# Kernel tuning notes

Hardware: AMD Instinct MI355X
Metric: run time of the kernel (lower is better)

Reference implementation:

```python
import jax, jax.numpy as jnp
import numpy as np
import math

NUM_HEADS = 12


def setup_inputs() -> dict:
    key = jax.random.key(0)
    ks = jax.random.split(key, 9)
    R, L, B, E = 128, 512, 1, 768
    s = 1.0 / math.sqrt(E)
    return {
        "x": jax.random.normal(ks[0], (R, L, B, E), dtype=jnp.float32),
        "wq": jax.random.normal(ks[1], (E, E), dtype=jnp.float32) * s,
        "bq": jax.random.normal(ks[2], (E,), dtype=jnp.float32) * 0.02,
        "wk": jax.random.normal(ks[3], (E, E), dtype=jnp.float32) * s,
        "bk": jax.random.normal(ks[4], (E,), dtype=jnp.float32) * 0.02,
        "wv": jax.random.normal(ks[5], (E, E), dtype=jnp.float32) * s,
        "bv": jax.random.normal(ks[6], (E,), dtype=jnp.float32) * 0.02,
        "wo": jax.random.normal(ks[7], (E, E), dtype=jnp.float32) * s,
        "bo": jax.random.normal(ks[8], (E,), dtype=jnp.float32) * 0.02,
    }


def reference(x, wq, bq, wk, bk, wv, bv, wo, bo):
    # x: [num_rows, num_cols, batch, embed_dim]
    R, L, B, E = x.shape
    H = NUM_HEADS
    D = E // H
    # scaling = head_dim**-0.5 / sqrt(num_rows)  (align_scaling)
    scaling = (D ** -0.5) / math.sqrt(R)

    q = (x @ wq.T + bq).reshape(R, L, B, H, D) * scaling
    k = (x @ wk.T + bk).reshape(R, L, B, H, D)
    v = (x @ wv.T + bv).reshape(R, L, B, H, D)

    # row attention: contract over rows r and head_dim d -> logits [h, n, i, j]
    attn_weights = jnp.einsum("rinhd,rjnhd->hnij", q, k)
    attn_probs = jax.nn.softmax(attn_weights, axis=-1)

    context = jnp.einsum("hnij,rjnhd->rinhd", attn_probs, v)
    context = context.reshape(R, L, B, E)
    output = context @ wo.T + bo
    return (output, attn_probs)
```

## Files before the change

kernel.cpp:

```cpp
#include <hip/hip_runtime.h>
#include <hip/hip_bf16.h>

typedef unsigned short u16;
typedef u16   u16x4 __attribute__((ext_vector_type(4)));
typedef u16   u16x8 __attribute__((ext_vector_type(8)));
typedef short bf16x8 __attribute__((ext_vector_type(8)));
typedef float f32x4 __attribute__((ext_vector_type(4)));

#define R_    128
#define L_    512
#define E_    768
#define H_    12
#define RD_   8192
#define M_    65536
#define OUT0_N 50331648
#define PART_ 3145728

__device__ __forceinline__ u16 rne_bf16(float f) {
  unsigned u = __builtin_bit_cast(unsigned, f);
  u += 0x7FFFu + ((u >> 16) & 1u);
  return (u16)(u >> 16);
}

__device__ __forceinline__ void gload_lds16(const u16* g, u16* l) {
  __builtin_amdgcn_global_load_lds(
      (const __attribute__((address_space(1))) void*)g,
      (__attribute__((address_space(3))) void*)l, 16, 0, 0);
}

__device__ __forceinline__ int xcd_remap(int d, int nwg) {
  return (d & 7) * (nwg >> 3) + (d >> 3);
}

__device__ __forceinline__ void gemm_core256(
    const u16* __restrict__ Ab, const u16* __restrict__ Bb,
    const int lda, const int ldb, const int K,
    u16* sm, f32x4 acc[8][4])
{
  const int t    = threadIdx.x;
  const int lane = t & 63;
  const int w    = t >> 6;
  const int wm   = (w >> 2) << 7;
  const int wn   = (w & 3) << 6;
  const int frow = lane & 15;

  const int srow  = t >> 2;
  const int gslot = (t & 3) ^ ((t >> 3) & 3);
  const u16* gA0 = Ab + (size_t)srow * lda + (gslot << 3);
  const u16* gA1 = Ab + (size_t)(srow + 128) * lda + (gslot << 3);
  const u16* gB0 = Bb + (size_t)srow * ldb + (gslot << 3);
  const u16* gB1 = Bb + (size_t)(srow + 128) * ldb + (gslot << 3);
  const int stg = t << 3;

  const int rdoff = (((lane >> 4) ^ ((lane >> 1) & 3)) << 3);

#define STAGE256(tt_, buf_)                                            \
  {                                                                    \
    const size_t ko_ = (size_t)(tt_) << 5;                             \
    gload_lds16(gA0 + ko_, (buf_) + stg);                              \
    gload_lds16(gA1 + ko_, (buf_) + 4096 + stg);                       \
    gload_lds16(gB0 + ko_, (buf_) + 8192 + stg);                       \
    gload_lds16(gB1 + ko_, (buf_) + 12288 + stg);                      \
  }

  const int nt = K >> 5;
  STAGE256(0, sm);
  asm volatile("s_waitcnt vmcnt(0)" ::: "memory");
  __builtin_amdgcn_s_barrier();

  for (int tt = 0; tt < nt; ++tt) {
    u16* bufc = sm + ((tt & 1) << 14);
    u16* bufn = sm + (((tt + 1) & 1) << 14);
    if (tt + 1 < nt) STAGE256(tt + 1, bufn);

    bf16x8 af[8], bff[4];
#pragma unroll
    for (int b = 0; b < 4; ++b)
      bff[b] = *(const bf16x8*)(bufc + 8192 + ((wn + b * 16 + frow) << 5) + rdoff);
#pragma unroll
    for (int a = 0; a < 8; ++a)
      af[a] = *(const bf16x8*)(bufc + ((wm + a * 16 + frow) << 5) + rdoff);

    __builtin_amdgcn_s_setprio(1);
#pragma unroll
    for (int a = 0; a < 8; ++a)
#pragma unroll
      for (int b = 0; b < 4; ++b)
        acc[a][b] = __builtin_amdgcn_mfma_f32_16x16x32_bf16(af[a], bff[b], acc[a][b], 0, 0, 0);
    __builtin_amdgcn_s_setprio(0);

    asm volatile("s_waitcnt vmcnt(0)" ::: "memory");
    __builtin_amdgcn_s_barrier();
  }
#undef STAGE256
}

#define EPILOGUE_IDX256                           \
  const int lane = threadIdx.x & 63;              \
  const int w    = threadIdx.x >> 6;              \
  const int wm   = (w >> 2) << 7;                 \
  const int wn   = (w & 3) << 6;                  \
  const int row4 = (lane >> 4) << 2;              \
  const int coll = lane & 15;

#define ACC_INIT256                               \
  f32x4 acc[8][4];                                \
  {                                               \
    f32x4 zz = {0.0f, 0.0f, 0.0f, 0.0f};          \
    _Pragma("unroll")                             \
    for (int a = 0; a < 8; ++a)                   \
      _Pragma("unroll")                           \
      for (int b = 0; b < 4; ++b) acc[a][b] = zz; \
  }

__device__ __forceinline__ void gemm_core(
    const u16* __restrict__ Ab, const u16* __restrict__ Bb,
    const int lda, const int ldb, const int K,
    u16* sm, f32x4 acc[4][4])
{
  const int t    = threadIdx.x;
  const int lane = t & 63;
  const int w    = t >> 6;
  const int wm   = (w >> 1) << 6;
  const int wn   = (w & 1) << 6;
  const int frow = lane & 15;

  const int srow = (w << 3) + (lane >> 3);
  const int scol = ((lane & 7) ^ (lane >> 3)) << 3;
  const u16* gA = Ab + (size_t)srow * lda + scol;
  const u16* gB = Bb + (size_t)srow * ldb + scol;
  const int stg_l = (w << 9) + (lane << 3);

#pragma unroll
  for (int j = 0; j < 4; ++j) {
    gload_lds16(gA + (size_t)(j << 5) * lda, sm + (j << 11) + stg_l);
    gload_lds16(gB + (size_t)(j << 5) * ldb, sm + 8192 + (j << 11) + stg_l);
  }

  const int nt = K >> 6;
  for (int tt = 0; tt < nt; ++tt) {
    const int cur = tt & 1;
    u16* bufc = sm + (cur << 14);
    u16* bufn = sm + ((cur ^ 1) << 14);
    __builtin_amdgcn_s_barrier();
    if (tt + 1 < nt) {
      const u16* gA1 = gA + ((size_t)(tt + 1) << 6);
      const u16* gB1 = gB + ((size_t)(tt + 1) << 6);
#pragma unroll
      for (int j = 0; j < 4; ++j) {
        gload_lds16(gA1 + (size_t)(j << 5) * lda, bufn + (j << 11) + stg_l);
        gload_lds16(gB1 + (size_t)(j << 5) * ldb, bufn + 8192 + (j << 11) + stg_l);
      }
      asm volatile("s_waitcnt vmcnt(8)" ::: "memory");
    } else {
      asm volatile("s_waitcnt vmcnt(0)" ::: "memory");
    }
    __builtin_amdgcn_s_barrier();
    const u16* sA = bufc;
    const u16* sB = bufc + 8192;
#pragma unroll
    for (int kk = 0; kk < 2; ++kk) {
      const int rdcol = (((kk << 2) + (lane >> 4)) ^ (lane & 7)) << 3;
      bf16x8 af[4], bff[4];
#pragma unroll
      for (int a = 0; a < 4; ++a)
        af[a] = *(const bf16x8*)(sA + ((wm + a * 16 + frow) << 6) + rdcol);
#pragma unroll
      for (int b = 0; b < 4; ++b)
        bff[b] = *(const bf16x8*)(sB + ((wn + b * 16 + frow) << 6) + rdcol);
#pragma unroll
      for (int a = 0; a < 4; ++a)
#pragma unroll
        for (int b = 0; b < 4; ++b)
          acc[a][b] = __builtin_amdgcn_mfma_f32_16x16x32_bf16(af[a], bff[b], acc[a][b], 0, 0, 0);
    }
  }
}

#define EPILOGUE_IDX                              \
  const int lane = threadIdx.x & 63;              \
  const int w    = threadIdx.x >> 6;              \
  const int wm   = (w >> 1) << 6;                 \
  const int wn   = (w & 1) << 6;                  \
  const int row4 = (lane >> 4) << 2;              \
  const int coll = lane & 15;

#define ACC_INIT                                  \
  f32x4 acc[4][4];                                \
  {                                               \
    f32x4 zz = {0.0f, 0.0f, 0.0f, 0.0f};          \
    _Pragma("unroll")                             \
    for (int a = 0; a < 4; ++a)                   \
      _Pragma("unroll")                           \
      for (int b = 0; b < 4; ++b) acc[a][b] = zz; \
  }

__global__ __launch_bounds__(512) void k_gemm_qkv(
    const u16* __restrict__ xbf, const u16* __restrict__ wqkv,
    const float* __restrict__ bq, const float* __restrict__ bk,
    const float* __restrict__ bv,
    u16* __restrict__ qt, u16* __restrict__ kt, u16* __restrict__ vt2,
    const float scaling)
{
  __shared__ __align__(16) u16 smem[32768];
  const int d0 = blockIdx.x + 9 * blockIdx.y;
  const int l  = xcd_remap(d0, 2304);
  const int bn = l % 9;
  const int bm = l / 9;
  ACC_INIT256;
  gemm_core256(xbf + (size_t)bm * 256 * E_, wqkv + (size_t)bn * 256 * E_,
               E_, E_, E_, smem, acc);
  EPILOGUE_IDX256;
  const int which = bn / 3;
  const int c0 = (bn % 3) << 8;
  const float* bias = (which == 0) ? bq : (which == 1) ? bk : bv;

  if (which < 2) {
    u16* dst = (which == 0) ? qt : kt;
    const float mult = (which == 0) ? scaling : 1.0f;
#pragma unroll
    for (int a = 0; a < 8; ++a) {
#pragma unroll
      for (int b = 0; b < 4; ++b) {
        const int c = c0 + wn + b * 16 + coll;
        const int h = c >> 6, d = c & 63;
        const float bias_v = bias[c];
#pragma unroll
        for (int r = 0; r < 4; ++r) {
          const int m = (bm << 8) + wm + a * 16 + row4 + r;
          const int rr = m >> 9, i = m & 511;
          const float v = (acc[a][b][r] + bias_v) * mult;
          dst[((size_t)(h * 512 + i) << 13) + (rr << 6) + d] = rne_bf16(v);
        }
      }
    }
  } else {
    const int rr = bm >> 1;
    const int j0 = (bm & 1) << 8;
    const int wq4 = w & 3;
    for (int p = 0; p < 4; ++p) {
      __syncthreads();
      if (wq4 == p) {
#pragma unroll
        for (int a = 0; a < 8; ++a) {
          const int ml = wm + a * 16 + row4;
#pragma unroll
          for (int b = 0; b < 4; ++b) {
            const int c = c0 + wn + b * 16 + coll;
            const int nl = b * 16 + coll;
            const float bias_v = bias[c];
            u16x4 pk;
#pragma unroll
            for (int r = 0; r < 4; ++r) pk[r] = rne_bf16(acc[a][b][r] + bias_v);
            *(u16x4*)(smem + nl * 264 + ml) = pk;
          }
        }
      }
      __syncthreads();
      for (int idx = threadIdx.x; idx < 2048; idx += 512) {
        const int nl = idx >> 5, seg = idx & 31;
        const int c = c0 + (p << 6) + nl;
        const int h = c >> 6, d = c & 63;
        u16x8 vdat = *(const u16x8*)(smem + nl * 264 + (seg << 3));
        *(u16x8*)(vt2 + ((size_t)((h << 13) + (rr << 6) + d) << 9) + j0 + (seg << 3)) = vdat;
      }
    }
  }
}

__global__ __launch_bounds__(256) void k_gemm_logits(
    const u16* __restrict__ qt, const u16* __restrict__ kt,
    float* __restrict__ lgp)
{
  __shared__ __align__(16) u16 smem[32768];
  const int d0 = blockIdx.x + 4 * blockIdx.y + 16 * blockIdx.z;
  const int l  = xcd_remap(d0, 768);
  const int bm = l & 3, bn = (l >> 2) & 3;
  const int hk = l >> 4;
  const int h  = hk >> 2, ks = hk & 3;
  ACC_INIT;
  const u16* A = qt + ((size_t)h << 22) + ((size_t)bm << 20) + (ks << 11);
  const u16* B = kt + ((size_t)h << 22) + ((size_t)bn << 20) + (ks << 11);
  gemm_core(A, B, RD_, RD_, 2048, smem, acc);
  EPILOGUE_IDX;
  float* dst = lgp + ((size_t)(ks * 12 + h) << 18);
#pragma unroll
  for (int a = 0; a < 4; ++a)
#pragma unroll
    for (int b = 0; b < 4; ++b) {
      const int j = bn * 128 + wn + b * 16 + coll;
#pragma unroll
      for (int r = 0; r < 4; ++r) {
        const int i = bm * 128 + wm + a * 16 + row4 + r;
        dst[((size_t)i << 9) + j] = acc[a][b][r];
      }
    }
}

__global__ __launch_bounds__(256) void k_softmax(
    const float* __restrict__ lgp, float* __restrict__ probs,
    u16* __restrict__ pbf)
{
  const int row = blockIdx.x;
  const size_t base = (size_t)row << 9;
  const int t = threadIdx.x;
  const int lane = t & 63, w = t >> 6;
  float x0 = (lgp[base + t]       + lgp[PART_ + base + t])
           + (lgp[2 * (size_t)PART_ + base + t]       + lgp[3 * (size_t)PART_ + base + t]);
  float x1 = (lgp[base + t + 256] + lgp[PART_ + base + t + 256])
           + (lgp[2 * (size_t)PART_ + base + t + 256] + lgp[3 * (size_t)PART_ + base + t + 256]);
  float m = fmaxf(x0, x1);
#pragma unroll
  for (int off = 32; off > 0; off >>= 1) m = fmaxf(m, __shfl_xor(m, off, 64));
  __shared__ float red[8];
  if (lane == 0) red[w] = m;
  __syncthreads();
  m = fmaxf(fmaxf(red[0], red[1]), fmaxf(red[2], red[3]));
  float e0 = __expf(x0 - m), e1 = __expf(x1 - m);
  float s = e0 + e1;
#pragma unroll
  for (int off = 32; off > 0; off >>= 1) s += __shfl_xor(s, off, 64);
  if (lane == 0) red[4 + w] = s;
  __syncthreads();
  s = (red[4] + red[5]) + (red[6] + red[7]);
  const float inv = 1.0f / s;
  const float p0 = e0 * inv, p1 = e1 * inv;
  probs[base + t] = p0;
  probs[base + t + 256] = p1;
  pbf[base + t]       = rne_bf16(p0);
  pbf[base + t + 256] = rne_bf16(p1);
}

__global__ __launch_bounds__(512) void k_gemm_ctx(
    const u16* __restrict__ pbf, const u16* __restrict__ vt2,
    u16* __restrict__ ctx)
{
  __shared__ __align__(16) u16 smem[32768];
  const int d0 = blockIdx.x + (blockIdx.y << 6);
  const int l  = xcd_remap(d0, 768);
  const int bm = l & 1, bn = (l >> 1) & 31, h = l >> 6;
  ACC_INIT256;
  const u16* A = pbf + ((size_t)h << 18) + ((size_t)bm << 17);
  const u16* B = vt2 + ((size_t)h << 22) + ((size_t)bn << 17);
  gemm_core256(A, B, 512, 512, 512, smem, acc);
  EPILOGUE_IDX256;
#pragma unroll
  for (int a = 0; a < 8; ++a)
#pragma unroll
    for (int b = 0; b < 4; ++b) {
      const int n = (bn << 8) + wn + b * 16 + coll;
      const int rr = n >> 6, d = n & 63;
#pragma unroll
      for (int r = 0; r < 4; ++r) {
        const int i = (bm << 8) + wm + a * 16 + row4 + r;
        ctx[(size_t)((rr << 9) + i) * E_ + (h << 6) + d] = rne_bf16(acc[a][b][r]);
      }
    }
}

__global__ __launch_bounds__(512) void k_gemm_out(
    const u16* __restrict__ ctx, const u16* __restrict__ wob,
    const float* __restrict__ bo, float* __restrict__ out0)
{
  __shared__ __align__(16) u16 smem[32768];
  const int d0 = blockIdx.x + 3 * blockIdx.y;
  const int l  = xcd_remap(d0, 768);
  const int bn = l % 3;
  const int bm = l / 3;
  ACC_INIT256;
  gemm_core256(ctx + (size_t)bm * 256 * E_, wob + (size_t)bn * 256 * E_,
               E_, E_, E_, smem, acc);
  EPILOGUE_IDX256;
#pragma unroll
  for (int a = 0; a < 8; ++a)
#pragma unroll
    for (int b = 0; b < 4; ++b) {
      const int n = (bn << 8) + wn + b * 16 + coll;
      const float bias_v = bo[n];
#pragma unroll
      for (int r = 0; r < 4; ++r) {
        const int m = (bm << 8) + wm + a * 16 + row4 + r;
        out0[(size_t)m * E_ + n] = acc[a][b][r] + bias_v;
      }
    }
}

__device__ __forceinline__ u16x4 cvt4(float4 v) {
  u16x4 o;
  o.x = rne_bf16(v.x); o.y = rne_bf16(v.y);
  o.z = rne_bf16(v.z); o.w = rne_bf16(v.w);
  return o;
}

__global__ __launch_bounds__(256) void k_cvt_x(
    const float4* __restrict__ src, u16x4* __restrict__ dst, const int n4)
{
  const int stride = gridDim.x * blockDim.x;
  for (int i = blockIdx.x * blockDim.x + threadIdx.x; i < n4; i += stride)
    dst[i] = cvt4(src[i]);
}

__global__ __launch_bounds__(256) void k_cvt_w(
    const float4* __restrict__ wq, const float4* __restrict__ wk,
    const float4* __restrict__ wv, const float4* __restrict__ wo,
    u16x4* __restrict__ wqkv, u16x4* __restrict__ wob)
{
  const int n4 = (E_ * E_) / 4;
  const int stride = gridDim.x * blockDim.x;
  for (int i = blockIdx.x * blockDim.x + threadIdx.x; i < n4; i += stride) {
    wqkv[i]            = cvt4(wq[i]);
    wqkv[n4 + i]       = cvt4(wk[i]);
    wqkv[2 * n4 + i]   = cvt4(wv[i]);
    wob[i]             = cvt4(wo[i]);
  }
}

__global__ void k_ws_too_small(float* out0) {
  if (threadIdx.x == 0 && blockIdx.x == 0) out0[0] = 1.0e9f;
}

extern "C" void kernel_launch(void* const* d_in, const int* in_sizes, int n_in,
                              void* d_out, int out_size, void* d_ws, size_t ws_size,
                              hipStream_t stream)
{
  const float* x  = (const float*)d_in[0];
  const float* wq = (const float*)d_in[1];
  const float* bq = (const float*)d_in[2];
  const float* wk = (const float*)d_in[3];
  const float* bk = (const float*)d_in[4];
  const float* wv = (const float*)d_in[5];
  const float* bv = (const float*)d_in[6];
  const float* wo = (const float*)d_in[7];
  const float* bo = (const float*)d_in[8];

  float* out0 = (float*)d_out;
  float* outp = out0 + (size_t)OUT0_N;

  const size_t off_xbf   = 0;
  const size_t off_qt    = 100663296;
  const size_t off_kt    = 201326592;
  const size_t off_vt    = 301989888;
  const size_t off_pbf   = 402653184;
  const size_t off_wqkv  = 408944640;
  const size_t off_wob   = 412483584;
  const size_t need      = 413663232;

  if (ws_size < need) {
    k_ws_too_small<<<1, 64, 0, stream>>>(out0);
    return;
  }

  char* ws = (char*)d_ws;
  u16* xbf  = (u16*)(ws + off_xbf);
  float* lgp = (float*)(ws + off_xbf);
  u16* qt   = (u16*)(ws + off_qt);
  u16* kt   = (u16*)(ws + off_kt);
  u16* vt2  = (u16*)(ws + off_vt);
  u16* pbf  = (u16*)(ws + off_pbf);
  u16* wqkv = (u16*)(ws + off_wqkv);
  u16* wob  = (u16*)(ws + off_wob);

  const float scaling = 0.011048543456039806f;

  k_cvt_x<<<2048, 256, 0, stream>>>((const float4*)x, (u16x4*)xbf, OUT0_N / 4);
  k_cvt_w<<<192, 256, 0, stream>>>((const float4*)wq, (const float4*)wk,
                                   (const float4*)wv, (const float4*)wo,
                                   (u16x4*)wqkv, (u16x4*)wob);
  k_gemm_qkv<<<dim3(9, 256), 512, 0, stream>>>(xbf, wqkv, bq, bk, bv,
                                               qt, kt, vt2, scaling);
  k_gemm_logits<<<dim3(4, 4, 48), 256, 0, stream>>>(qt, kt, lgp);
  k_softmax<<<6144, 256, 0, stream>>>(lgp, outp, pbf);
  k_gemm_ctx<<<dim3(64, 12), 512, 0, stream>>>(pbf, vt2, xbf );
  k_gemm_out<<<dim3(3, 256), 512, 0, stream>>>(xbf, wob, bo, out0);
}
```

Baseline: 646.0 us.

## Deepen GEMM K-tile to 64 and interleave staged loads with MFMA sub-phases

The shared 256x256 GEMM core now uses a K-step of 64 instead of 32, doubling LDS per buffer (128 KB total for double buffering), with an 8-slot XOR swizzle. Each iteration is split into four compute phases, and the next tile's global-to-LDS loads are issued in quarters between them with partial vmcnt waits. The aim is to halve the number of loop iterations and overlap memory traffic with MFMA work more finely. The extra LDS limits occupancy to one block per CU, and the added barriers cost synchronisation.

```diff
diff --git a/kernel.cpp b/kernel.cpp
--- a/kernel.cpp
+++ b/kernel.cpp
@@ -44,55 +44,100 @@
   const int wn   = (w & 3) << 6;
   const int frow = lane & 15;
 
-  const int srow  = t >> 2;
-  const int gslot = (t & 3) ^ ((t >> 3) & 3);
-  const u16* gA0 = Ab + (size_t)srow * lda + (gslot << 3);
-  const u16* gA1 = Ab + (size_t)(srow + 128) * lda + (gslot << 3);
-  const u16* gB0 = Bb + (size_t)srow * ldb + (gslot << 3);
-  const u16* gB1 = Bb + (size_t)(srow + 128) * ldb + (gslot << 3);
+  const int crow  = t >> 3;
+  const int gslot = (t & 7) ^ (crow & 7);
+  const u16* gA = Ab + (size_t)crow * lda + (gslot << 3);
+  const u16* gB = Bb + (size_t)crow * ldb + (gslot << 3);
   const int stg = t << 3;
 
-  const int rdoff = (((lane >> 4) ^ ((lane >> 1) & 3)) << 3);
-
-#define STAGE256(tt_, buf_)                                            \
-  {                                                                    \
-    const size_t ko_ = (size_t)(tt_) << 5;                             \
-    gload_lds16(gA0 + ko_, (buf_) + stg);                              \
-    gload_lds16(gA1 + ko_, (buf_) + 4096 + stg);                       \
-    gload_lds16(gB0 + ko_, (buf_) + 8192 + stg);                       \
-    gload_lds16(gB1 + ko_, (buf_) + 12288 + stg);                      \
-  }
-
-  const int nt = K >> 5;
-  STAGE256(0, sm);
-  asm volatile("s_waitcnt vmcnt(0)" ::: "memory");
+  const int rd0 = (((lane >> 4)    ) ^ (lane & 7)) << 3;
+  const int rd1 = (((lane >> 4) | 4) ^ (lane & 7)) << 3;
+
+#define STG_A(c_, buf_, ko_) \
+  gload_lds16(gA + (ko_) + (size_t)((c_) << 6) * lda, (buf_) + ((c_) << 12) + stg)
+#define STG_B(c_, buf_, ko_) \
+  gload_lds16(gB + (ko_) + (size_t)((c_) << 6) * ldb, (buf_) + 16384 + ((c_) << 12) + stg)
+
+  const int nt = K >> 6;
+  STG_B(0, sm, 0); STG_B(1, sm, 0); STG_B(2, sm, 0); STG_B(3, sm, 0);
+  STG_A(0, sm, 0); STG_A(2, sm, 0); STG_A(1, sm, 0); STG_A(3, sm, 0);
+  asm volatile("s_waitcnt vmcnt(2)" ::: "memory");
   __builtin_amdgcn_s_barrier();
 
   for (int tt = 0; tt < nt; ++tt) {
-    u16* bufc = sm + ((tt & 1) << 14);
-    u16* bufn = sm + (((tt + 1) & 1) << 14);
-    if (tt + 1 < nt) STAGE256(tt + 1, bufn);
-
-    bf16x8 af[8], bff[4];
+    u16* bufc = sm + ((tt & 1) << 15);
+    u16* bufn = sm + (((tt + 1) & 1) << 15);
+    const bool st = (tt + 1 < nt);
+    const int ko = (tt + 1) << 6;
+
+    bf16x8 af[4], bff[4];
 #pragma unroll
     for (int b = 0; b < 4; ++b)
-      bff[b] = *(const bf16x8*)(bufc + 8192 + ((wn + b * 16 + frow) << 5) + rdoff);
-#pragma unroll
-    for (int a = 0; a < 8; ++a)
-      af[a] = *(const bf16x8*)(bufc + ((wm + a * 16 + frow) << 5) + rdoff);
-
+      bff[b] = *(const bf16x8*)(bufc + 16384 + ((wn + b * 16 + frow) << 6) + rd0);
+#pragma unroll
+    for (int a = 0; a < 4; ++a)
+      af[a] = *(const bf16x8*)(bufc + ((wm + a * 16 + frow) << 6) + rd0);
+    if (st) { STG_B(0, bufn, ko); STG_B(1, bufn, ko); }
+    __builtin_amdgcn_s_barrier();
     __builtin_amdgcn_s_setprio(1);
 #pragma unroll
-    for (int a = 0; a < 8; ++a)
+    for (int a = 0; a < 4; ++a)
 #pragma unroll
       for (int b = 0; b < 4; ++b)
         acc[a][b] = __builtin_amdgcn_mfma_f32_16x16x32_bf16(af[a], bff[b], acc[a][b], 0, 0, 0);
     __builtin_amdgcn_s_setprio(0);
-
-    asm volatile("s_waitcnt vmcnt(0)" ::: "memory");
-    __builtin_amdgcn_s_barrier();
-  }
-#undef STAGE256
+    if (st) asm volatile("s_waitcnt vmcnt(2)" ::: "memory");
+    else    asm volatile("s_waitcnt vmcnt(0)" ::: "memory");
+    __builtin_amdgcn_s_barrier();
+
+#pragma unroll
+    for (int a = 0; a < 4; ++a)
+      af[a] = *(const bf16x8*)(bufc + ((wm + (a + 4) * 16 + frow) << 6) + rd0);
+    if (st) { STG_B(2, bufn, ko); STG_B(3, bufn, ko); }
+    __builtin_amdgcn_s_barrier();
+    __builtin_amdgcn_s_setprio(1);
+#pragma unroll
+    for (int a = 0; a < 4; ++a)
+#pragma unroll
+      for (int b = 0; b < 4; ++b)
+        acc[a + 4][b] = __builtin_amdgcn_mfma_f32_16x16x32_bf16(af[a], bff[b], acc[a + 4][b], 0, 0, 0);
+    __builtin_amdgcn_s_setprio(0);
+    __builtin_amdgcn_s_barrier();
+
+#pragma unroll
+    for (int b = 0; b < 4; ++b)
+      bff[b] = *(const bf16x8*)(bufc + 16384 + ((wn + b * 16 + frow) << 6) + rd1);
+#pragma unroll
+    for (int a = 0; a < 4; ++a)
+      af[a] = *(const bf16x8*)(bufc + ((wm + a * 16 + frow) << 6) + rd1);
+    if (st) { STG_A(0, bufn, ko); STG_A(2, bufn, ko); }
+    __builtin_amdgcn_s_barrier();
+    __builtin_amdgcn_s_setprio(1);
+#pragma unroll
+    for (int a = 0; a < 4; ++a)
+#pragma unroll
+      for (int b = 0; b < 4; ++b)
+        acc[a][b] = __builtin_amdgcn_mfma_f32_16x16x32_bf16(af[a], bff[b], acc[a][b], 0, 0, 0);
+    __builtin_amdgcn_s_setprio(0);
+    __builtin_amdgcn_s_barrier();
+
+#pragma unroll
+    for (int a = 0; a < 4; ++a)
+      af[a] = *(const bf16x8*)(bufc + ((wm + (a + 4) * 16 + frow) << 6) + rd1);
+    if (st) { STG_A(1, bufn, ko); STG_A(3, bufn, ko); }
+    __builtin_amdgcn_s_barrier();
+    __builtin_amdgcn_s_setprio(1);
+#pragma unroll
+    for (int a = 0; a < 4; ++a)
+#pragma unroll
+      for (int b = 0; b < 4; ++b)
+        acc[a + 4][b] = __builtin_amdgcn_mfma_f32_16x16x32_bf16(af[a], bff[b], acc[a + 4][b], 0, 0, 0);
+    __builtin_amdgcn_s_setprio(0);
+    if (st) asm volatile("s_waitcnt vmcnt(2)" ::: "memory");
+    __builtin_amdgcn_s_barrier();
+  }
+#undef STG_A
+#undef STG_B
 }
 
 #define EPILOGUE_IDX256                           \
@@ -202,7 +247,7 @@
     u16* __restrict__ qt, u16* __restrict__ kt, u16* __restrict__ vt2,
     const float scaling)
 {
-  __shared__ __align__(16) u16 smem[32768];
+  __shared__ __align__(16) u16 smem[65536];
   const int d0 = blockIdx.x + 9 * blockIdx.y;
   const int l  = xcd_remap(d0, 2304);
   const int bn = l % 9;
@@ -335,7 +380,7 @@
     const u16* __restrict__ pbf, const u16* __restrict__ vt2,
     u16* __restrict__ ctx)
 {
-  __shared__ __align__(16) u16 smem[32768];
+  __shared__ __align__(16) u16 smem[65536];
   const int d0 = blockIdx.x + (blockIdx.y << 6);
   const int l  = xcd_remap(d0, 768);
   const int bm = l & 1, bn = (l >> 1) & 31, h = l >> 6;
@@ -362,7 +407,7 @@
     const u16* __restrict__ ctx, const u16* __restrict__ wob,
     const float* __restrict__ bo, float* __restrict__ out0)
 {
-  __shared__ __align__(16) u16 smem[32768];
+  __shared__ __align__(16) u16 smem[65536];
   const int d0 = blockIdx.x + 3 * blockIdx.y;
   const int l  = xcd_remap(d0, 768);
   const int bn = l % 3;
```

Measured after the change: 601.3 us. 6.9% less time.
